# Performance work log

Hardware: AMD Instinct MI355X
Metric: run time of the kernel (lower is better)

Reference implementation:

```python
import jax, jax.numpy as jnp
import numpy as np

B, N, K1, M, D = 8, 4096, 17, 2, 256
NT = B * N          # total nodes
EPS = 1e-5          # PyG LayerNorm default eps


def setup_inputs() -> dict:
    key = jax.random.key(0)
    ks = jax.random.split(key, 13)
    s = 1.0 / np.sqrt(D)
    return {
        "x": jax.random.normal(ks[0], (NT, M, D), jnp.float32),
        "knn_edges": jax.random.randint(ks[1], (B, N, K1), 0, N),
        "edge_mask": jax.random.bernoulli(ks[2], 0.9, (B, N, K1)),
        "W0": jax.random.normal(ks[3], (D, D), jnp.float32) * s,
        "b0": jnp.zeros((D,), jnp.float32),
        "g0": jnp.ones((D,), jnp.float32),
        "be0": jnp.zeros((D,), jnp.float32),
        "a0": jnp.full((1,), 0.25, jnp.float32),
        "W1": jax.random.normal(ks[4], (D, D), jnp.float32) * s,
        "b1": jnp.zeros((D,), jnp.float32),
        "g1": jnp.ones((D,), jnp.float32),
        "be1": jnp.zeros((D,), jnp.float32),
        "a1": jnp.full((1,), 0.25, jnp.float32),
    }


def knn_to_edges(knn_edges, edge_mask):
    # drop self column 0, add per-graph batch offsets; keep fixed E with 0/1 weights
    e = knn_edges[:, :, 1:]                       # [B, N, K]
    m = edge_mask[:, :, 1:]
    off = (jnp.arange(B) * N)[:, None, None]      # [B,1,1]
    src = jnp.broadcast_to(jnp.arange(N)[None, :, None] + off, e.shape).reshape(-1)
    dst = (e + off).reshape(-1)
    w = m.reshape(-1).astype(jnp.float32)         # invalid edges -> weight 0
    return src, dst, w


def gcn_conv(h_in, W, b, src, dst, w):
    # PyG GCNConv: add self-loops (weight 1), symmetric normalization
    h = h_in @ W                                            # [NT, D]
    deg = jax.ops.segment_sum(w, dst, num_segments=NT) + 1.0
    dinv = jax.lax.rsqrt(deg)                               # [NT]
    norm = dinv[src] * w * dinv[dst]                        # [E]
    agg = jax.ops.segment_sum(norm[:, None] * h[src], dst, num_segments=NT)
    agg = agg + (dinv * dinv)[:, None] * h                  # self-loop term
    return agg + b


def graph_layernorm(x, g, b):
    # PyG LayerNorm mode='graph', batch=None: normalize over all nodes+features
    xc = x - jnp.mean(x)
    std = jnp.sqrt(jnp.mean(xc * xc))
    return g * (xc / (std + EPS)) + b


def prelu(x, a):
    return jnp.where(x >= 0, x, a * x)


def reference(x, knn_edges, edge_mask, W0, b0, g0, be0, a0, W1, b1, g1, be1, a1):
    src, dst, w = knn_to_edges(knn_edges, edge_mask)
    h = x[:, 0, :]                                          # [NT, D]
    for (W, b, g, be, a) in ((W0, b0, g0, be0, a0), (W1, b1, g1, be1, a1)):
        h = gcn_conv(h, W, b, src, dst, w)
        h = graph_layernorm(h, g, be)
        h = prelu(h, a)
    return h
```

## Files before the change

### kernel.cpp

```cpp
#include <hip/hip_runtime.h>
#include <hip/hip_bf16.h>
#include <stdint.h>

#define B_   8
#define N_   4096
#define K1_  17
#define D_   256
#define NT_  (B_*N_)
#define E16_ (NT_*16)
#define NP_  (NT_*D_)
#define EPS_ 1e-5f

typedef __attribute__((ext_vector_type(8))) short short8v;
typedef __attribute__((ext_vector_type(4))) short short4v;
typedef __attribute__((ext_vector_type(4))) float f32x4;

__device__ __forceinline__ unsigned short f2bfu(float f){
  unsigned u = __float_as_uint(f);
  unsigned r = (u + 0x7FFFu + ((u>>16)&1u)) >> 16;
  return (unsigned short)r;
}
__device__ __forceinline__ short f2bf(float f){ return (short)f2bfu(f); }
__device__ __forceinline__ unsigned pkbf(float lo, float hi){
  return (unsigned)f2bfu(lo) | ((unsigned)f2bfu(hi) << 16);
}
__device__ __forceinline__ float bf2f(short s){
  return __uint_as_float(((unsigned)(unsigned short)s) << 16);
}
__device__ __forceinline__ void unpack2(unsigned u, float& lo, float& hi){
  lo = __uint_as_float(u << 16);
  hi = __uint_as_float(u & 0xFFFF0000u);
}

__global__ __launch_bounds__(256) void k_prep(const float* __restrict__ W0,
                                              const float* __restrict__ W1,
                                              short* __restrict__ Wt0,
                                              short* __restrict__ Wt1,
                                              int* __restrict__ degcnt,
                                              const unsigned int* __restrict__ mw,
                                              int* __restrict__ flag){
  if (blockIdx.x < 128){
    const float* W  = (blockIdx.x & 1) ? W1  : W0;
    short*       Wt = (blockIdx.x & 1) ? Wt1 : Wt0;
    int tile = blockIdx.x >> 1;
    int ti = tile >> 3, tj = tile & 7;
    __shared__ float sm[32][33];
    int r = threadIdx.x >> 5, c = threadIdx.x & 31;
    #pragma unroll
    for (int i=0;i<4;i++)
      sm[r + i*8][c] = W[(ti*32 + r + i*8)*256 + tj*32 + c];
    __syncthreads();
    #pragma unroll
    for (int i=0;i<4;i++){
      int rr = r + i*8;
      Wt[(size_t)(tj*32 + rr)*256 + ti*32 + c] = f2bf(sm[c][rr]);
    }
  } else {
    int ib = blockIdx.x - 128;
    int i  = ib*256 + threadIdx.x;
    degcnt[i] = 0;
    if (ib == 0){
      __shared__ int s_int, s_f32;
      if (threadIdx.x==0){ s_int=1; s_f32=1; }
      __syncthreads();
      int bad_i=0, bad_f=0;
      #pragma unroll
      for (int j=0;j<4;j++){
        unsigned w = mw[threadIdx.x*4 + j];
        if (!(w==0u || w==1u))          bad_i=1;
        if (!(w==0u || w==0x3F800000u)) bad_f=1;
      }
      if (bad_i) atomicAnd(&s_int, 0);
      if (bad_f) atomicAnd(&s_f32, 0);
      __syncthreads();
      if (threadIdx.x==0) *flag = s_int ? 0 : (s_f32 ? 1 : 2);
    }
  }
}

__device__ __forceinline__ bool mask_at(const void* maskp, int f, int idx){
  if (f==0) return ((const int*)maskp)[idx] != 0;
  if (f==1) return ((const float*)maskp)[idx] != 0.0f;
  return ((const unsigned char*)maskp)[idx] != 0;
}

__global__ void k_deg(const int* __restrict__ knn, const void* __restrict__ maskp,
                      const int* __restrict__ flag, int* __restrict__ degcnt){
  int f = *flag;
  int e = blockIdx.x*blockDim.x + threadIdx.x;
  if (e >= E16_) return;
  int node = e >> 4;
  int k    = (e & 15) + 1;
  int idx  = node*K1_ + k;
  if (mask_at(maskp, f, idx)){
    int b   = node >> 12;
    int dst = knn[idx] + (b<<12);
    atomicAdd(&degcnt[dst], 1);
  }
}

__global__ void k_scan(const int* __restrict__ degcnt, int* __restrict__ rowptr,
                       int* __restrict__ fillptr, float* __restrict__ dinv){
  __shared__ int wsum[16];
  int t = threadIdx.x;
  int lane = t & 63, wid = t >> 6;
  int base = t*32;
  int loc[32]; int tot = 0;
  #pragma unroll
  for (int i=0;i<32;i++){ loc[i] = degcnt[base+i]; tot += loc[i]; }
  int inc = tot;
  #pragma unroll
  for (int off=1; off<64; off<<=1){
    int v = __shfl_up(inc, off, 64);
    if (lane >= off) inc += v;
  }
  if (lane == 63) wsum[wid] = inc;
  __syncthreads();
  int woff = 0;
  #pragma unroll
  for (int i=0;i<16;i++) if (i < wid) woff += wsum[i];
  int run = woff + inc - tot;
  #pragma unroll
  for (int i=0;i<32;i++){
    int v = base+i;
    rowptr[v]  = run;
    fillptr[v] = run;
    dinv[v]    = rsqrtf((float)loc[i] + 1.0f);
    run += loc[i];
  }
  if (t==1023) rowptr[NT_] = run;
}

__global__ __launch_bounds__(256, 3) void k_gemm_x_fill(const float* __restrict__ X,
                                                        const short* __restrict__ Wt,
                                                        short* __restrict__ C,
                                                        const int* __restrict__ knn,
                                                        const void* __restrict__ maskp,
                                                        const int* __restrict__ flag,
                                                        int* __restrict__ fillptr,
                                                        int* __restrict__ col){
  __shared__ short lA[128*64];
  __shared__ short lB[128*64];
  if (blockIdx.x >= 512){
    int f = *flag;
    int e = (blockIdx.x - 512)*256 + threadIdx.x;
    int node = e >> 4;
    int k    = (e & 15) + 1;
    int idx  = node*K1_ + k;
    if (mask_at(maskp, f, idx)){
      int b   = node >> 12;
      int dst = knn[idx] + (b<<12);
      int pos = atomicAdd(&fillptr[dst], 1);
      col[pos] = node;
    }
    return;
  }
  int lb     = (int)(blockIdx.x & 7)*64 + (int)(blockIdx.x >> 3);
  int rowblk = lb >> 1, half = lb & 1;
  int rowB = rowblk*128, colB = half*128;

  int t    = threadIdx.x;
  int wave = t >> 6, lane = t & 63;
  int lr   = lane & 15, qg = lane >> 4;
  int wr   = wave >> 1, wc = wave & 1;

  f32x4 acc[4][4];
  #pragma unroll
  for (int m=0;m<4;m++)
    #pragma unroll
    for (int n=0;n<4;n++) acc[m][n] = (f32x4){0.f,0.f,0.f,0.f};

  int srow[4], sch[4];
  #pragma unroll
  for (int i=0;i<4;i++){ int e = t + i*256; srow[i] = e>>3; sch[i] = e&7; }

  float4 rax[4], ray[4]; uint4 rb[4];
  #pragma unroll
  for (int i=0;i<4;i++){
    const float* ap = X + (size_t)(rowB+srow[i])*512 + sch[i]*8;
    rax[i] = *(const float4*)ap;
    ray[i] = *(const float4*)(ap+4);
    rb[i]  = *(const uint4*)(Wt + (size_t)(colB+srow[i])*256 + sch[i]*8);
  }

  for (int kc=0; kc<4; kc++){
    if (kc) __syncthreads();
    #pragma unroll
    for (int i=0;i<4;i++){
      int ph = srow[i]*8 + (sch[i] ^ (srow[i]&7));
      uint4 cv;
      cv.x = pkbf(rax[i].x, rax[i].y); cv.y = pkbf(rax[i].z, rax[i].w);
      cv.z = pkbf(ray[i].x, ray[i].y); cv.w = pkbf(ray[i].z, ray[i].w);
      *(uint4*)(lA + ph*8) = cv;
      *(uint4*)(lB + ph*8) = rb[i];
    }
    __syncthreads();
    if (kc < 3){
      #pragma unroll
      for (int i=0;i<4;i++){
        const float* ap = X + (size_t)(rowB+srow[i])*512 + (kc+1)*64 + sch[i]*8;
        rax[i] = *(const float4*)ap;
        ray[i] = *(const float4*)(ap+4);
        rb[i]  = *(const uint4*)(Wt + (size_t)(colB+srow[i])*256 + (kc+1)*64 + sch[i]*8);
      }
    }
    #pragma unroll
    for (int ks=0; ks<2; ks++){
      short8v af[4], bfr[4];
      #pragma unroll
      for (int m=0;m<4;m++){
        int row = wr*64 + m*16 + lr;
        af[m] = *(const short8v*)(lA + (row*8 + ((ks*4+qg) ^ (row&7)))*8);
      }
      #pragma unroll
      for (int n=0;n<4;n++){
        int coln = wc*64 + n*16 + lr;
        bfr[n] = *(const short8v*)(lB + (coln*8 + ((ks*4+qg) ^ (coln&7)))*8);
      }
      #pragma unroll
      for (int m=0;m<4;m++)
        #pragma unroll
        for (int n=0;n<4;n++)
          acc[m][n] = __builtin_amdgcn_mfma_f32_16x16x32_bf16(af[m], bfr[n], acc[m][n], 0, 0, 0);
    }
  }

  #pragma unroll
  for (int m=0;m<4;m++){
    int crow = rowB + wr*64 + m*16 + qg*4;
    #pragma unroll
    for (int n=0;n<4;n++){
      int ccol = colB + wc*64 + n*16 + lr;
      #pragma unroll
      for (int r=0;r<4;r++)
        C[(size_t)(crow + r)*256 + ccol] = f2bf(acc[m][n][r]);
    }
  }
}

__global__ __launch_bounds__(256, 3) void k_gemm_n(const unsigned* __restrict__ BaggU,
                                                   const float* __restrict__ g,
                                                   const float* __restrict__ be,
                                                   const float* __restrict__ aP,
                                                   const float* __restrict__ stats,
                                                   const short* __restrict__ Wt,
                                                   short* __restrict__ C){
  float mean = stats[0], inv = stats[1], a = aP[0];
  __shared__ short lA[128*64];
  __shared__ short lB[128*64];
  int lb     = (int)(blockIdx.x & 7)*64 + (int)(blockIdx.x >> 3);
  int rowblk = lb >> 1, half = lb & 1;
  int rowB = rowblk*128, colB = half*128;

  int t    = threadIdx.x;
  int wave = t >> 6, lane = t & 63;
  int lr   = lane & 15, qg = lane >> 4;
  int wr   = wave >> 1, wc = wave & 1;

  f32x4 acc[4][4];
  #pragma unroll
  for (int m=0;m<4;m++)
    #pragma unroll
    for (int n=0;n<4;n++) acc[m][n] = (f32x4){0.f,0.f,0.f,0.f};

  int srow[4], sch[4];
  #pragma unroll
  for (int i=0;i<4;i++){ int e = t + i*256; srow[i] = e>>3; sch[i] = e&7; }

  uint4 ra[4], rb[4];
  #pragma unroll
  for (int i=0;i<4;i++){
    ra[i] = *(const uint4*)(BaggU + (size_t)(rowB+srow[i])*128 + sch[i]*4);
    rb[i] = *(const uint4*)(Wt + (size_t)(colB+srow[i])*256 + sch[i]*8);
  }

  for (int kc=0; kc<4; kc++){
    if (kc) __syncthreads();
    #pragma unroll
    for (int i=0;i<4;i++){
      int ph = srow[i]*8 + (sch[i] ^ (srow[i]&7));
      int c0 = kc*64 + sch[i]*8;
      float4 g0 = *(const float4*)&g[c0],  g1 = *(const float4*)&g[c0+4];
      float4 e0 = *(const float4*)&be[c0], e1 = *(const float4*)&be[c0+4];
      float v[8];
      unpack2(ra[i].x, v[0], v[1]); unpack2(ra[i].y, v[2], v[3]);
      unpack2(ra[i].z, v[4], v[5]); unpack2(ra[i].w, v[6], v[7]);
      float gg[8] = {g0.x,g0.y,g0.z,g0.w,g1.x,g1.y,g1.z,g1.w};
      float eb[8] = {e0.x,e0.y,e0.z,e0.w,e1.x,e1.y,e1.z,e1.w};
      float o[8];
      #pragma unroll
      for (int j=0;j<8;j++){
        float tt = gg[j]*((v[j]-mean)*inv) + eb[j];
        o[j] = tt>=0.f ? tt : a*tt;
      }
      uint4 cv;
      cv.x = pkbf(o[0],o[1]); cv.y = pkbf(o[2],o[3]);
      cv.z = pkbf(o[4],o[5]); cv.w = pkbf(o[6],o[7]);
      *(uint4*)(lA + ph*8) = cv;
      *(uint4*)(lB + ph*8) = rb[i];
    }
    __syncthreads();
    if (kc < 3){
      #pragma unroll
      for (int i=0;i<4;i++){
        ra[i] = *(const uint4*)(BaggU + (size_t)(rowB+srow[i])*128 + (kc+1)*32 + sch[i]*4);
        rb[i] = *(const uint4*)(Wt + (size_t)(colB+srow[i])*256 + (kc+1)*64 + sch[i]*8);
      }
    }
    #pragma unroll
    for (int ks=0; ks<2; ks++){
      short8v af[4], bfr[4];
      #pragma unroll
      for (int m=0;m<4;m++){
        int row = wr*64 + m*16 + lr;
        af[m] = *(const short8v*)(lA + (row*8 + ((ks*4+qg) ^ (row&7)))*8);
      }
      #pragma unroll
      for (int n=0;n<4;n++){
        int coln = wc*64 + n*16 + lr;
        bfr[n] = *(const short8v*)(lB + (coln*8 + ((ks*4+qg) ^ (coln&7)))*8);
      }
      #pragma unroll
      for (int m=0;m<4;m++)
        #pragma unroll
        for (int n=0;n<4;n++)
          acc[m][n] = __builtin_amdgcn_mfma_f32_16x16x32_bf16(af[m], bfr[n], acc[m][n], 0, 0, 0);
    }
  }

  #pragma unroll
  for (int m=0;m<4;m++){
    int crow = rowB + wr*64 + m*16 + qg*4;
    #pragma unroll
    for (int n=0;n<4;n++){
      int ccol = colB + wc*64 + n*16 + lr;
      #pragma unroll
      for (int r=0;r<4;r++)
        C[(size_t)(crow + r)*256 + ccol] = f2bf(acc[m][n][r]);
    }
  }
}

__global__ __launch_bounds__(256) void k_agg(const short* __restrict__ Ab,
    const int* __restrict__ rowptr, const int* __restrict__ col,
    const float* __restrict__ dinv, const float* __restrict__ bvec,
    unsigned* __restrict__ outU, float* __restrict__ partS, float* __restrict__ partQ){
  int bid  = (int)(blockIdx.x & 7) * 512 + (int)(blockIdx.x >> 3);
  int node = bid*8 + (threadIdx.x >> 5);
  int sub  = threadIdx.x & 31;
  int c0   = sub*8;
  float dv = dinv[node];

  float acc[8];
  {
    short8v s = *(const short8v*)&Ab[(size_t)node*256 + c0];
    #pragma unroll
    for (int i=0;i<8;i++) acc[i] = dv * bf2f(s[i]);
  }
  int j0 = rowptr[node], j1 = rowptr[node+1];
  for (int base=j0; base<j1; base+=32){
    int n = j1 - base; n = n < 32 ? n : 32;
    int   myc = (sub < n) ? col[base+sub] : 0;
    float myd = (sub < n) ? dinv[myc]     : 0.f;
    for (int j=0;j<n;j++){
      int   s  = __shfl(myc, j, 32);
      float ds = __shfl(myd, j, 32);
      short8v nb = *(const short8v*)&Ab[(size_t)s*256 + c0];
      #pragma unroll
      for (int i=0;i<8;i++) acc[i] += ds * bf2f(nb[i]);
    }
  }
  float sum=0.f, sq=0.f;
  float o[8];
  #pragma unroll
  for (int i=0;i<8;i++){
    float v = dv*acc[i] + bvec[c0+i];
    o[i] = v;
    sum += v; sq += v*v;
  }
  uint4 ov;
  ov.x = pkbf(o[0],o[1]); ov.y = pkbf(o[2],o[3]);
  ov.z = pkbf(o[4],o[5]); ov.w = pkbf(o[6],o[7]);
  *(uint4*)&outU[(size_t)node*128 + sub*4] = ov;

  #pragma unroll
  for (int off=16; off>0; off>>=1){
    sum += __shfl_down(sum, off, 32);
    sq  += __shfl_down(sq,  off, 32);
  }
  __shared__ float ls1[8], ls2[8];
  if (sub==0){ ls1[threadIdx.x>>5]=sum; ls2[threadIdx.x>>5]=sq; }
  __syncthreads();
  if (threadIdx.x==0){
    float a=0.f, b=0.f;
    #pragma unroll
    for (int i=0;i<8;i++){ a+=ls1[i]; b+=ls2[i]; }
    partS[bid]=a; partQ[bid]=b;
  }
}

__global__ void k_stats(const float* __restrict__ partS, const float* __restrict__ partQ,
                        float* __restrict__ stats){
  __shared__ double s1[1024], s2[1024];
  int t = threadIdx.x;
  double a=0.0, b=0.0;
  for (int i=t; i<4096; i+=1024){ a += (double)partS[i]; b += (double)partQ[i]; }
  s1[t]=a; s2[t]=b; __syncthreads();
  for (int off=512; off>0; off>>=1){
    if (t<off){ s1[t]+=s1[t+off]; s2[t]+=s2[t+off]; }
    __syncthreads();
  }
  if (t==0){
    double mean = s1[0] / (double)NP_;
    double var  = s2[0] / (double)NP_ - mean*mean;
    var = var > 0.0 ? var : 0.0;
    stats[0] = (float)mean;
    stats[1] = (float)(1.0 / (sqrt(var) + (double)EPS_));
  }
}

__global__ __launch_bounds__(256) void k_norm_f32(const unsigned* __restrict__ inU,
    const float* __restrict__ g, const float* __restrict__ be,
    const float* __restrict__ aP, const float* __restrict__ stats,
    float* __restrict__ out){
  float mean = stats[0], inv = stats[1], a = aP[0];
  int gid   = blockIdx.x*256 + threadIdx.x;
  int base8 = gid*8;
  int c0    = base8 & (D_-1);
  uint4 vin = *(const uint4*)&inU[gid*4];
  float4 g0 = *(const float4*)&g[c0],  g1 = *(const float4*)&g[c0+4];
  float4 e0 = *(const float4*)&be[c0], e1 = *(const float4*)&be[c0+4];
  float v[8];
  unpack2(vin.x, v[0], v[1]); unpack2(vin.y, v[2], v[3]);
  unpack2(vin.z, v[4], v[5]); unpack2(vin.w, v[6], v[7]);
  float gg[8] = {g0.x,g0.y,g0.z,g0.w,g1.x,g1.y,g1.z,g1.w};
  float eb[8] = {e0.x,e0.y,e0.z,e0.w,e1.x,e1.y,e1.z,e1.w};
  f32x4 o0, o1;
  #pragma unroll
  for (int i=0;i<8;i++){
    float tt = gg[i]*((v[i]-mean)*inv) + eb[i];
    tt = tt>=0.f ? tt : a*tt;
    if (i<4) o0[i] = tt; else o1[i-4] = tt;
  }
  *(f32x4*)&out[base8]     = o0;
  *(f32x4*)&out[base8 + 4] = o1;
}


extern "C" void kernel_launch(void* const* d_in, const int* in_sizes, int n_in,
                              void* d_out, int out_size, void* d_ws, size_t ws_size,
                              hipStream_t stream){
  const float* x    = (const float*)d_in[0];
  const int*   knn  = (const int*)  d_in[1];
  const void*  mask =               d_in[2];
  const float* W0   = (const float*)d_in[3];
  const float* b0   = (const float*)d_in[4];
  const float* g0   = (const float*)d_in[5];
  const float* be0  = (const float*)d_in[6];
  const float* a0   = (const float*)d_in[7];
  const float* W1   = (const float*)d_in[8];
  const float* b1   = (const float*)d_in[9];
  const float* g1   = (const float*)d_in[10];
  const float* be1  = (const float*)d_in[11];
  const float* a1   = (const float*)d_in[12];
  float* out = (float*)d_out;

  char* w = (char*)d_ws;
  size_t off = 0;
  auto alloc = [&](size_t bytes)->void*{
    void* p = w + off; off = (off + bytes + 255) & ~(size_t)255; return p;
  };
  int*      degcnt  = (int*)     alloc(NT_*4);
  int*      rowptr  = (int*)     alloc((NT_+1)*4);
  int*      fillptr = (int*)     alloc(NT_*4);
  int*      col     = (int*)     alloc(E16_*4);
  float*    dinv    = (float*)   alloc(NT_*4);
  float*    partS   = (float*)   alloc(4096*4);
  float*    partQ   = (float*)   alloc(4096*4);
  float*    stats   = (float*)   alloc(4*4);
  int*      flag    = (int*)     alloc(4);
  short*    Ab      = (short*)   alloc((size_t)NP_*2);
  unsigned* Bagg    = (unsigned*)alloc((size_t)NP_*2);
  short*    Wt0     = (short*)   alloc(256*256*2);
  short*    Wt1     = (short*)   alloc(256*256*2);

  hipLaunchKernelGGL(k_prep,  dim3(256),      dim3(256), 0, stream, W0, W1, Wt0, Wt1,
                     degcnt, (const unsigned int*)mask, flag);
  hipLaunchKernelGGL(k_deg,   dim3(E16_/256), dim3(256), 0, stream, knn, mask, flag, degcnt);
  hipLaunchKernelGGL(k_scan,  dim3(1),        dim3(1024),0, stream, degcnt, rowptr, fillptr, dinv);

  hipLaunchKernelGGL(k_gemm_x_fill, dim3(2560), dim3(256), 0, stream, x, Wt0, Ab,
                     knn, mask, flag, fillptr, col);
  hipLaunchKernelGGL(k_agg,    dim3(NT_/8),   dim3(256), 0, stream, Ab, rowptr, col, dinv, b0, Bagg, partS, partQ);
  hipLaunchKernelGGL(k_stats,  dim3(1),       dim3(1024),0, stream, partS, partQ, stats);

  hipLaunchKernelGGL(k_gemm_n, dim3(512),     dim3(256), 0, stream, Bagg, g0, be0, a0, stats, Wt1, Ab);
  hipLaunchKernelGGL(k_agg,    dim3(NT_/8),   dim3(256), 0, stream, Ab, rowptr, col, dinv, b1, Bagg, partS, partQ);
  hipLaunchKernelGGL(k_stats,  dim3(1),       dim3(1024),0, stream, partS, partQ, stats);
  hipLaunchKernelGGL(k_norm_f32, dim3(NP_/2048), dim3(256), 0, stream, Bagg, g1, be1, a1, stats, out);
}
```

Before: 159.8 us.

## Use 512-thread GEMM blocks and stage bf16 output through LDS for coalesced stores

```diff
diff --git a/kernel.cpp b/kernel.cpp
--- a/kernel.cpp
+++ b/kernel.cpp
@@ -131,7 +131,7 @@
   if (t==1023) rowptr[NT_] = run;
 }
 
-__global__ __launch_bounds__(256, 3) void k_gemm_x_fill(const float* __restrict__ X,
+__global__ __launch_bounds__(512, 4) void k_gemm_x_fill(const float* __restrict__ X,
                                                         const short* __restrict__ Wt,
                                                         short* __restrict__ C,
                                                         const int* __restrict__ knn,
@@ -139,11 +139,10 @@
                                                         const int* __restrict__ flag,
                                                         int* __restrict__ fillptr,
                                                         int* __restrict__ col){
-  __shared__ short lA[128*64];
-  __shared__ short lB[128*64];
+  __shared__ short lds[2*128*64];
   if (blockIdx.x >= 512){
     int f = *flag;
-    int e = (blockIdx.x - 512)*256 + threadIdx.x;
+    int e = (int)(blockIdx.x - 512)*512 + threadIdx.x;
     int node = e >> 4;
     int k    = (e & 15) + 1;
     int idx  = node*K1_ + k;
@@ -155,6 +154,8 @@
     }
     return;
   }
+  short* lA = lds;
+  short* lB = lds + 128*64;
   int lb     = (int)(blockIdx.x & 7)*64 + (int)(blockIdx.x >> 3);
   int rowblk = lb >> 1, half = lb & 1;
   int rowB = rowblk*128, colB = half*128;
@@ -162,21 +163,21 @@
   int t    = threadIdx.x;
   int wave = t >> 6, lane = t & 63;
   int lr   = lane & 15, qg = lane >> 4;
-  int wr   = wave >> 1, wc = wave & 1;
-
-  f32x4 acc[4][4];
+  int wr   = wave >> 2, wc = wave & 3;
+
+  f32x4 acc[4][2];
   #pragma unroll
   for (int m=0;m<4;m++)
     #pragma unroll
-    for (int n=0;n<4;n++) acc[m][n] = (f32x4){0.f,0.f,0.f,0.f};
-
-  int srow[4], sch[4];
-  #pragma unroll
-  for (int i=0;i<4;i++){ int e = t + i*256; srow[i] = e>>3; sch[i] = e&7; }
-
-  float4 rax[4], ray[4]; uint4 rb[4];
-  #pragma unroll
-  for (int i=0;i<4;i++){
+    for (int n=0;n<2;n++) acc[m][n] = (f32x4){0.f,0.f,0.f,0.f};
+
+  int srow[2], sch[2];
+  #pragma unroll
+  for (int i=0;i<2;i++){ int e = t + i*512; srow[i] = e>>3; sch[i] = e&7; }
+
+  float4 rax[2], ray[2]; uint4 rb[2];
+  #pragma unroll
+  for (int i=0;i<2;i++){
     const float* ap = X + (size_t)(rowB+srow[i])*512 + sch[i]*8;
     rax[i] = *(const float4*)ap;
     ray[i] = *(const float4*)(ap+4);
@@ -186,7 +187,7 @@
   for (int kc=0; kc<4; kc++){
     if (kc) __syncthreads();
     #pragma unroll
-    for (int i=0;i<4;i++){
+    for (int i=0;i<2;i++){
       int ph = srow[i]*8 + (sch[i] ^ (srow[i]&7));
       uint4 cv;
       cv.x = pkbf(rax[i].x, rax[i].y); cv.y = pkbf(rax[i].z, rax[i].w);
@@ -197,7 +198,7 @@
     __syncthreads();
     if (kc < 3){
       #pragma unroll
-      for (int i=0;i<4;i++){
+      for (int i=0;i<2;i++){
         const float* ap = X + (size_t)(rowB+srow[i])*512 + (kc+1)*64 + sch[i]*8;
         rax[i] = *(const float4*)ap;
         ray[i] = *(const float4*)(ap+4);
@@ -206,39 +207,51 @@
     }
     #pragma unroll
     for (int ks=0; ks<2; ks++){
-      short8v af[4], bfr[4];
+      short8v af[4], bfr[2];
       #pragma unroll
       for (int m=0;m<4;m++){
         int row = wr*64 + m*16 + lr;
         af[m] = *(const short8v*)(lA + (row*8 + ((ks*4+qg) ^ (row&7)))*8);
       }
       #pragma unroll
-      for (int n=0;n<4;n++){
-        int coln = wc*64 + n*16 + lr;
+      for (int n=0;n<2;n++){
+        int coln = wc*32 + n*16 + lr;
         bfr[n] = *(const short8v*)(lB + (coln*8 + ((ks*4+qg) ^ (coln&7)))*8);
       }
       #pragma unroll
       for (int m=0;m<4;m++)
         #pragma unroll
-        for (int n=0;n<4;n++)
+        for (int n=0;n<2;n++)
           acc[m][n] = __builtin_amdgcn_mfma_f32_16x16x32_bf16(af[m], bfr[n], acc[m][n], 0, 0, 0);
     }
   }
 
+  __syncthreads();
   #pragma unroll
   for (int m=0;m<4;m++){
-    int crow = rowB + wr*64 + m*16 + qg*4;
-    #pragma unroll
-    for (int n=0;n<4;n++){
-      int ccol = colB + wc*64 + n*16 + lr;
-      #pragma unroll
-      for (int r=0;r<4;r++)
-        C[(size_t)(crow + r)*256 + ccol] = f2bf(acc[m][n][r]);
-    }
-  }
-}
-
-__global__ __launch_bounds__(256, 3) void k_gemm_n(const unsigned* __restrict__ BaggU,
+    int rloc = wr*64 + m*16 + qg*4;
+    #pragma unroll
+    for (int n=0;n<2;n++){
+      int cloc = wc*32 + n*16 + lr;
+      int cch  = cloc >> 3, cin = cloc & 7;
+      #pragma unroll
+      for (int r=0;r<4;r++){
+        int row = rloc + r;
+        lds[row*128 + ((cch ^ (row&7))<<3) + cin] = f2bf(acc[m][n][r]);
+      }
+    }
+  }
+  __syncthreads();
+  #pragma unroll
+  for (int i=0;i<4;i++){
+    int e = t + i*512;
+    int row = e >> 4, chunk = e & 15;
+    uint4 v = *(const uint4*)(lds + row*128 + ((chunk ^ (row&7))<<3));
+    *(uint4*)(C + (size_t)(rowB+row)*256 + colB + chunk*8) = v;
+  }
+}
+
+__global__ __launch_bounds__(512, 4) void k_gemm_n(const unsigned* __restrict__ BaggU,
                                                    const float* __restrict__ g,
                                                    const float* __restrict__ be,
                                                    const float* __restrict__ aP,
@@ -246,8 +259,9 @@
                                                    const short* __restrict__ Wt,
                                                    short* __restrict__ C){
   float mean = stats[0], inv = stats[1], a = aP[0];
-  __shared__ short lA[128*64];
-  __shared__ short lB[128*64];
+  __shared__ short lds[2*128*64];
+  short* lA = lds;
+  short* lB = lds + 128*64;
   int lb     = (int)(blockIdx.x & 7)*64 + (int)(blockIdx.x >> 3);
   int rowblk = lb >> 1, half = lb & 1;
   int rowB = rowblk*128, colB = half*128;
@@ -255,21 +269,21 @@
   int t    = threadIdx.x;
   int wave = t >> 6, lane = t & 63;
   int lr   = lane & 15, qg = lane >> 4;
-  int wr   = wave >> 1, wc = wave & 1;
-
-  f32x4 acc[4][4];
+  int wr   = wave >> 2, wc = wave & 3;
+
+  f32x4 acc[4][2];
   #pragma unroll
   for (int m=0;m<4;m++)
     #pragma unroll
-    for (int n=0;n<4;n++) acc[m][n] = (f32x4){0.f,0.f,0.f,0.f};
-
-  int srow[4], sch[4];
-  #pragma unroll
-  for (int i=0;i<4;i++){ int e = t + i*256; srow[i] = e>>3; sch[i] = e&7; }
-
-  uint4 ra[4], rb[4];
-  #pragma unroll
-  for (int i=0;i<4;i++){
+    for (int n=0;n<2;n++) acc[m][n] = (f32x4){0.f,0.f,0.f,0.f};
+
+  int srow[2], sch[2];
+  #pragma unroll
+  for (int i=0;i<2;i++){ int e = t + i*512; srow[i] = e>>3; sch[i] = e&7; }
+
+  uint4 ra[2], rb[2];
+  #pragma unroll
+  for (int i=0;i<2;i++){
     ra[i] = *(const uint4*)(BaggU + (size_t)(rowB+srow[i])*128 + sch[i]*4);
     rb[i] = *(const uint4*)(Wt + (size_t)(colB+srow[i])*256 + sch[i]*8);
   }
@@ -277,7 +291,7 @@
   for (int kc=0; kc<4; kc++){
     if (kc) __syncthreads();
     #pragma unroll
-    for (int i=0;i<4;i++){
+    for (int i=0;i<2;i++){
       int ph = srow[i]*8 + (sch[i] ^ (srow[i]&7));
       int c0 = kc*64 + sch[i]*8;
       float4 g0 = *(const float4*)&g[c0],  g1 = *(const float4*)&g[c0+4];
@@ -302,42 +316,54 @@
     __syncthreads();
     if (kc < 3){
       #pragma unroll
-      for (int i=0;i<4;i++){
+      for (int i=0;i<2;i++){
         ra[i] = *(const uint4*)(BaggU + (size_t)(rowB+srow[i])*128 + (kc+1)*32 + sch[i]*4);
         rb[i] = *(const uint4*)(Wt + (size_t)(colB+srow[i])*256 + (kc+1)*64 + sch[i]*8);
       }
     }
     #pragma unroll
     for (int ks=0; ks<2; ks++){
-      short8v af[4], bfr[4];
+      short8v af[4], bfr[2];
       #pragma unroll
       for (int m=0;m<4;m++){
         int row = wr*64 + m*16 + lr;
         af[m] = *(const short8v*)(lA + (row*8 + ((ks*4+qg) ^ (row&7)))*8);
       }
       #pragma unroll
-      for (int n=0;n<4;n++){
-        int coln = wc*64 + n*16 + lr;
+      for (int n=0;n<2;n++){
+        int coln = wc*32 + n*16 + lr;
         bfr[n] = *(const short8v*)(lB + (coln*8 + ((ks*4+qg) ^ (coln&7)))*8);
       }
       #pragma unroll
       for (int m=0;m<4;m++)
         #pragma unroll
-        for (int n=0;n<4;n++)
+        for (int n=0;n<2;n++)
           acc[m][n] = __builtin_amdgcn_mfma_f32_16x16x32_bf16(af[m], bfr[n], acc[m][n], 0, 0, 0);
     }
   }
 
+  __syncthreads();
   #pragma unroll
   for (int m=0;m<4;m++){
-    int crow = rowB + wr*64 + m*16 + qg*4;
-    #pragma unroll
-    for (int n=0;n<4;n++){
-      int ccol = colB + wc*64 + n*16 + lr;
-      #pragma unroll
-      for (int r=0;r<4;r++)
-        C[(size_t)(crow + r)*256 + ccol] = f2bf(acc[m][n][r]);
-    }
+    int rloc = wr*64 + m*16 + qg*4;
+    #pragma unroll
+    for (int n=0;n<2;n++){
+      int cloc = wc*32 + n*16 + lr;
+      int cch  = cloc >> 3, cin = cloc & 7;
+      #pragma unroll
+      for (int r=0;r<4;r++){
+        int row = rloc + r;
+        lds[row*128 + ((cch ^ (row&7))<<3) + cin] = f2bf(acc[m][n][r]);
+      }
+    }
+  }
+  __syncthreads();
+  #pragma unroll
+  for (int i=0;i<4;i++){
+    int e = t + i*512;
+    int row = e >> 4, chunk = e & 15;
+    uint4 v = *(const uint4*)(lds + row*128 + ((chunk ^ (row&7))<<3));
+    *(uint4*)(C + (size_t)(rowB+row)*256 + colB + chunk*8) = v;
   }
 }
 
@@ -489,12 +515,12 @@
   hipLaunchKernelGGL(k_deg,   dim3(E16_/256), dim3(256), 0, stream, knn, mask, flag, degcnt);
   hipLaunchKernelGGL(k_scan,  dim3(1),        dim3(1024),0, stream, degcnt, rowptr, fillptr, dinv);
 
-  hipLaunchKernelGGL(k_gemm_x_fill, dim3(2560), dim3(256), 0, stream, x, Wt0, Ab,
+  hipLaunchKernelGGL(k_gemm_x_fill, dim3(1536), dim3(512), 0, stream, x, Wt0, Ab,
                      knn, mask, flag, fillptr, col);
   hipLaunchKernelGGL(k_agg,    dim3(NT_/8),   dim3(256), 0, stream, Ab, rowptr, col, dinv, b0, Bagg, partS, partQ);
   hipLaunchKernelGGL(k_stats,  dim3(1),       dim3(1024),0, stream, partS, partQ, stats);
 
-  hipLaunchKernelGGL(k_gemm_n, dim3(512),     dim3(256), 0, stream, Bagg, g0, be0, a0, stats, Wt1, Ab);
+  hipLaunchKernelGGL(k_gemm_n, dim3(512),     dim3(512), 0, stream, Bagg, g0, be0, a0, stats, Wt1, Ab);
   hipLaunchKernelGGL(k_agg,    dim3(NT_/8),   dim3(256), 0, stream, Ab, rowptr, col, dinv, b1, Bagg, partS, partQ);
   hipLaunchKernelGGL(k_stats,  dim3(1),       dim3(1024),0, stream, partS, partQ, stats);
   hipLaunchKernelGGL(k_norm_f32, dim3(NP_/2048), dim3(256), 0, stream, Bagg, g1, be1, a1, stats, out);
```

After: 161.4 us. Within noise of the previous version (+1.0%).

## Fuse graph-norm stats reduction into consumers and widen GEMM tiles to full N

Applied to the files above, without the earlier changes.

```diff
diff --git a/kernel.cpp b/kernel.cpp
--- a/kernel.cpp
+++ b/kernel.cpp
@@ -12,7 +12,6 @@
 #define EPS_ 1e-5f
 
 typedef __attribute__((ext_vector_type(8))) short short8v;
-typedef __attribute__((ext_vector_type(4))) short short4v;
 typedef __attribute__((ext_vector_type(4))) float f32x4;
 
 __device__ __forceinline__ unsigned short f2bfu(float f){
@@ -131,7 +130,47 @@
   if (t==1023) rowptr[NT_] = run;
 }
 
-__global__ __launch_bounds__(256, 3) void k_gemm_x_fill(const float* __restrict__ X,
+__device__ __forceinline__ void g_mfma4(const short* lA, const short* lB,
+                                        int wr, int wc, int lr, int qg,
+                                        f32x4 (&acc)[4][4]){
+  #pragma unroll
+  for (int ks=0; ks<2; ks++){
+    short8v af[4], bfr[4];
+    #pragma unroll
+    for (int m=0;m<4;m++){
+      int row = wr*64 + m*16 + lr;
+      af[m] = *(const short8v*)(lA + (row*8 + ((ks*4+qg) ^ (row&7)))*8);
+    }
+    #pragma unroll
+    for (int n=0;n<4;n++){
+      int coln = wc*64 + n*16 + lr;
+      bfr[n] = *(const short8v*)(lB + (coln*8 + ((ks*4+qg) ^ (coln&7)))*8);
+    }
+    #pragma unroll
+    for (int m=0;m<4;m++)
+      #pragma unroll
+      for (int n=0;n<4;n++)
+        acc[m][n] = __builtin_amdgcn_mfma_f32_16x16x32_bf16(af[m], bfr[n], acc[m][n], 0, 0, 0);
+  }
+}
+
+__device__ __forceinline__ void g_cstore(short* __restrict__ C, int rowB,
+                                         int wr, int wc, int lr, int qg,
+                                         const f32x4 (&acc)[4][4]){
+  #pragma unroll
+  for (int m=0;m<4;m++){
+    int crow = rowB + wr*64 + m*16 + qg*4;
+    #pragma unroll
+    for (int n=0;n<4;n++){
+      int ccol = wc*64 + n*16 + lr;
+      #pragma unroll
+      for (int r=0;r<4;r++)
+        C[(size_t)(crow + r)*256 + ccol] = f2bf(acc[m][n][r]);
+    }
+  }
+}
+
+__global__ __launch_bounds__(512, 4) void k_gemm_x_fill(const float* __restrict__ X,
                                                         const short* __restrict__ Wt,
                                                         short* __restrict__ C,
                                                         const int* __restrict__ knn,
@@ -140,10 +179,10 @@
                                                         int* __restrict__ fillptr,
                                                         int* __restrict__ col){
   __shared__ short lA[128*64];
-  __shared__ short lB[128*64];
-  if (blockIdx.x >= 512){
+  __shared__ short lB[256*64];
+  if (blockIdx.x >= 256){
     int f = *flag;
-    int e = (blockIdx.x - 512)*256 + threadIdx.x;
+    int e = (int)(blockIdx.x - 256)*512 + threadIdx.x;
     int node = e >> 4;
     int k    = (e & 15) + 1;
     int idx  = node*K1_ + k;
@@ -155,14 +194,13 @@
     }
     return;
   }
-  int lb     = (int)(blockIdx.x & 7)*64 + (int)(blockIdx.x >> 3);
-  int rowblk = lb >> 1, half = lb & 1;
-  int rowB = rowblk*128, colB = half*128;
+  int lb   = (int)(blockIdx.x & 7)*32 + (int)(blockIdx.x >> 3);
+  int rowB = lb*128;
 
   int t    = threadIdx.x;
   int wave = t >> 6, lane = t & 63;
   int lr   = lane & 15, qg = lane >> 4;
-  int wr   = wave >> 1, wc = wave & 1;
+  int wr   = wave >> 2, wc = wave & 3;
 
   f32x4 acc[4][4];
   #pragma unroll
@@ -170,92 +208,98 @@
     #pragma unroll
     for (int n=0;n<4;n++) acc[m][n] = (f32x4){0.f,0.f,0.f,0.f};
 
-  int srow[4], sch[4];
-  #pragma unroll
-  for (int i=0;i<4;i++){ int e = t + i*256; srow[i] = e>>3; sch[i] = e&7; }
-
-  float4 rax[4], ray[4]; uint4 rb[4];
-  #pragma unroll
-  for (int i=0;i<4;i++){
-    const float* ap = X + (size_t)(rowB+srow[i])*512 + sch[i]*8;
+  int saA[2], scA[2], saB[4], scB[4];
+  #pragma unroll
+  for (int i=0;i<2;i++){ int e = t + i*512; saA[i] = e>>3; scA[i] = e&7; }
+  #pragma unroll
+  for (int i=0;i<4;i++){ int e = t + i*512; saB[i] = e>>3; scB[i] = e&7; }
+
+  float4 rax[2], ray[2]; uint4 rb[4];
+  #pragma unroll
+  for (int i=0;i<2;i++){
+    const float* ap = X + (size_t)(rowB+saA[i])*512 + scA[i]*8;
     rax[i] = *(const float4*)ap;
     ray[i] = *(const float4*)(ap+4);
-    rb[i]  = *(const uint4*)(Wt + (size_t)(colB+srow[i])*256 + sch[i]*8);
-  }
+  }
+  #pragma unroll
+  for (int i=0;i<4;i++)
+    rb[i] = *(const uint4*)(Wt + (size_t)saB[i]*256 + scB[i]*8);
 
   for (int kc=0; kc<4; kc++){
     if (kc) __syncthreads();
     #pragma unroll
-    for (int i=0;i<4;i++){
-      int ph = srow[i]*8 + (sch[i] ^ (srow[i]&7));
+    for (int i=0;i<2;i++){
+      int ph = saA[i]*8 + (scA[i] ^ (saA[i]&7));
       uint4 cv;
       cv.x = pkbf(rax[i].x, rax[i].y); cv.y = pkbf(rax[i].z, rax[i].w);
       cv.z = pkbf(ray[i].x, ray[i].y); cv.w = pkbf(ray[i].z, ray[i].w);
       *(uint4*)(lA + ph*8) = cv;
+    }
+    #pragma unroll
+    for (int i=0;i<4;i++){
+      int ph = saB[i]*8 + (scB[i] ^ (saB[i]&7));
       *(uint4*)(lB + ph*8) = rb[i];
     }
     __syncthreads();
     if (kc < 3){
       #pragma unroll
-      for (int i=0;i<4;i++){
-        const float* ap = X + (size_t)(rowB+srow[i])*512 + (kc+1)*64 + sch[i]*8;
+      for (int i=0;i<2;i++){
+        const float* ap = X + (size_t)(rowB+saA[i])*512 + (kc+1)*64 + scA[i]*8;
         rax[i] = *(const float4*)ap;
         ray[i] = *(const float4*)(ap+4);
-        rb[i]  = *(const uint4*)(Wt + (size_t)(colB+srow[i])*256 + (kc+1)*64 + sch[i]*8);
       }
-    }
-    #pragma unroll
-    for (int ks=0; ks<2; ks++){
-      short8v af[4], bfr[4];
-      #pragma unroll
-      for (int m=0;m<4;m++){
-        int row = wr*64 + m*16 + lr;
-        af[m] = *(const short8v*)(lA + (row*8 + ((ks*4+qg) ^ (row&7)))*8);
-      }
-      #pragma unroll
-      for (int n=0;n<4;n++){
-        int coln = wc*64 + n*16 + lr;
-        bfr[n] = *(const short8v*)(lB + (coln*8 + ((ks*4+qg) ^ (coln&7)))*8);
-      }
-      #pragma unroll
-      for (int m=0;m<4;m++)
-        #pragma unroll
-        for (int n=0;n<4;n++)
-          acc[m][n] = __builtin_amdgcn_mfma_f32_16x16x32_bf16(af[m], bfr[n], acc[m][n], 0, 0, 0);
-    }
-  }
-
-  #pragma unroll
-  for (int m=0;m<4;m++){
-    int crow = rowB + wr*64 + m*16 + qg*4;
-    #pragma unroll
-    for (int n=0;n<4;n++){
-      int ccol = colB + wc*64 + n*16 + lr;
-      #pragma unroll
-      for (int r=0;r<4;r++)
-        C[(size_t)(crow + r)*256 + ccol] = f2bf(acc[m][n][r]);
-    }
-  }
-}
-
-__global__ __launch_bounds__(256, 3) void k_gemm_n(const unsigned* __restrict__ BaggU,
+      #pragma unroll
+      for (int i=0;i<4;i++)
+        rb[i] = *(const uint4*)(Wt + (size_t)saB[i]*256 + (kc+1)*64 + scB[i]*8);
+    }
+    g_mfma4(lA, lB, wr, wc, lr, qg, acc);
+  }
+  g_cstore(C, rowB, wr, wc, lr, qg, acc);
+}
+
+__global__ __launch_bounds__(512, 4) void k_gemm_n(const unsigned* __restrict__ BaggU,
                                                    const float* __restrict__ g,
                                                    const float* __restrict__ be,
                                                    const float* __restrict__ aP,
-                                                   const float* __restrict__ stats,
+                                                   const float* __restrict__ partS,
+                                                   const float* __restrict__ partQ,
                                                    const short* __restrict__ Wt,
                                                    short* __restrict__ C){
-  float mean = stats[0], inv = stats[1], a = aP[0];
   __shared__ short lA[128*64];
-  __shared__ short lB[128*64];
-  int lb     = (int)(blockIdx.x & 7)*64 + (int)(blockIdx.x >> 3);
-  int rowblk = lb >> 1, half = lb & 1;
-  int rowB = rowblk*128, colB = half*128;
+  __shared__ short lB[256*64];
+  float mean, inv;
+  {
+    double* sS = (double*)lA;
+    double* sQ = (double*)(lA + 4096);
+    double a=0.0, b=0.0;
+    for (int i=threadIdx.x; i<4096; i+=512){ a += (double)partS[i]; b += (double)partQ[i]; }
+    sS[threadIdx.x]=a; sQ[threadIdx.x]=b;
+    __syncthreads();
+    for (int off=256; off>0; off>>=1){
+      if ((int)threadIdx.x < off){ sS[threadIdx.x]+=sS[threadIdx.x+off]; sQ[threadIdx.x]+=sQ[threadIdx.x+off]; }
+      __syncthreads();
+    }
+    if (threadIdx.x==0){
+      double m   = sS[0] / (double)NP_;
+      double var = sQ[0] / (double)NP_ - m*m;
+      var = var > 0.0 ? var : 0.0;
+      ((float*)lA)[0] = (float)m;
+      ((float*)lA)[1] = (float)(1.0 / (sqrt(var) + (double)EPS_));
+    }
+    __syncthreads();
+    mean = ((float*)lA)[0];
+    inv  = ((float*)lA)[1];
+    __syncthreads();
+  }
+  float a = aP[0];
+
+  int lb   = (int)(blockIdx.x & 7)*32 + (int)(blockIdx.x >> 3);
+  int rowB = lb*128;
 
   int t    = threadIdx.x;
   int wave = t >> 6, lane = t & 63;
   int lr   = lane & 15, qg = lane >> 4;
-  int wr   = wave >> 1, wc = wave & 1;
+  int wr   = wave >> 2, wc = wave & 3;
 
   f32x4 acc[4][4];
   #pragma unroll
@@ -263,23 +307,26 @@
     #pragma unroll
     for (int n=0;n<4;n++) acc[m][n] = (f32x4){0.f,0.f,0.f,0.f};
 
-  int srow[4], sch[4];
-  #pragma unroll
-  for (int i=0;i<4;i++){ int e = t + i*256; srow[i] = e>>3; sch[i] = e&7; }
-
-  uint4 ra[4], rb[4];
-  #pragma unroll
-  for (int i=0;i<4;i++){
-    ra[i] = *(const uint4*)(BaggU + (size_t)(rowB+srow[i])*128 + sch[i]*4);
-    rb[i] = *(const uint4*)(Wt + (size_t)(colB+srow[i])*256 + sch[i]*8);
-  }
+  int saA[2], scA[2], saB[4], scB[4];
+  #pragma unroll
+  for (int i=0;i<2;i++){ int e = t + i*512; saA[i] = e>>3; scA[i] = e&7; }
+  #pragma unroll
+  for (int i=0;i<4;i++){ int e = t + i*512; saB[i] = e>>3; scB[i] = e&7; }
+
+  uint4 ra[2], rb[4];
+  #pragma unroll
+  for (int i=0;i<2;i++)
+    ra[i] = *(const uint4*)(BaggU + (size_t)(rowB+saA[i])*128 + scA[i]*4);
+  #pragma unroll
+  for (int i=0;i<4;i++)
+    rb[i] = *(const uint4*)(Wt + (size_t)saB[i]*256 + scB[i]*8);
 
   for (int kc=0; kc<4; kc++){
     if (kc) __syncthreads();
     #pragma unroll
-    for (int i=0;i<4;i++){
-      int ph = srow[i]*8 + (sch[i] ^ (srow[i]&7));
-      int c0 = kc*64 + sch[i]*8;
+    for (int i=0;i<2;i++){
+      int ph = saA[i]*8 + (scA[i] ^ (saA[i]&7));
+      int c0 = kc*64 + scA[i]*8;
       float4 g0 = *(const float4*)&g[c0],  g1 = *(const float4*)&g[c0+4];
       float4 e0 = *(const float4*)&be[c0], e1 = *(const float4*)&be[c0+4];
       float v[8];
@@ -297,48 +344,24 @@
       cv.x = pkbf(o[0],o[1]); cv.y = pkbf(o[2],o[3]);
       cv.z = pkbf(o[4],o[5]); cv.w = pkbf(o[6],o[7]);
       *(uint4*)(lA + ph*8) = cv;
+    }
+    #pragma unroll
+    for (int i=0;i<4;i++){
+      int ph = saB[i]*8 + (scB[i] ^ (saB[i]&7));
       *(uint4*)(lB + ph*8) = rb[i];
     }
     __syncthreads();
     if (kc < 3){
       #pragma unroll
-      for (int i=0;i<4;i++){
-        ra[i] = *(const uint4*)(BaggU + (size_t)(rowB+srow[i])*128 + (kc+1)*32 + sch[i]*4);
-        rb[i] = *(const uint4*)(Wt + (size_t)(colB+srow[i])*256 + (kc+1)*64 + sch[i]*8);
-      }
-    }
-    #pragma unroll
-    for (int ks=0; ks<2; ks++){
-      short8v af[4], bfr[4];
-      #pragma unroll
-      for (int m=0;m<4;m++){
-        int row = wr*64 + m*16 + lr;
-        af[m] = *(const short8v*)(lA + (row*8 + ((ks*4+qg) ^ (row&7)))*8);
-      }
-      #pragma unroll
-      for (int n=0;n<4;n++){
-        int coln = wc*64 + n*16 + lr;
-        bfr[n] = *(const short8v*)(lB + (coln*8 + ((ks*4+qg) ^ (coln&7)))*8);
-      }
-      #pragma unroll
-      for (int m=0;m<4;m++)
-        #pragma unroll
-        for (int n=0;n<4;n++)
-          acc[m][n] = __builtin_amdgcn_mfma_f32_16x16x32_bf16(af[m], bfr[n], acc[m][n], 0, 0, 0);
-    }
-  }
-
-  #pragma unroll
-  for (int m=0;m<4;m++){
-    int crow = rowB + wr*64 + m*16 + qg*4;
-    #pragma unroll
-    for (int n=0;n<4;n++){
-      int ccol = colB + wc*64 + n*16 + lr;
-      #pragma unroll
-      for (int r=0;r<4;r++)
-        C[(size_t)(crow + r)*256 + ccol] = f2bf(acc[m][n][r]);
-    }
-  }
+      for (int i=0;i<2;i++)
+        ra[i] = *(const uint4*)(BaggU + (size_t)(rowB+saA[i])*128 + (kc+1)*32 + scA[i]*4);
+      #pragma unroll
+      for (int i=0;i<4;i++)
+        rb[i] = *(const uint4*)(Wt + (size_t)saB[i]*256 + (kc+1)*64 + scB[i]*8);
+    }
+    g_mfma4(lA, lB, wr, wc, lr, qg, acc);
+  }
+  g_cstore(C, rowB, wr, wc, lr, qg, acc);
 }
 
 __global__ __launch_bounds__(256) void k_agg(const short* __restrict__ Ab,
@@ -399,51 +422,54 @@
   }
 }
 
-__global__ void k_stats(const float* __restrict__ partS, const float* __restrict__ partQ,
-                        float* __restrict__ stats){
-  __shared__ double s1[1024], s2[1024];
-  int t = threadIdx.x;
-  double a=0.0, b=0.0;
-  for (int i=t; i<4096; i+=1024){ a += (double)partS[i]; b += (double)partQ[i]; }
-  s1[t]=a; s2[t]=b; __syncthreads();
-  for (int off=512; off>0; off>>=1){
-    if (t<off){ s1[t]+=s1[t+off]; s2[t]+=s2[t+off]; }
-    __syncthreads();
-  }
-  if (t==0){
-    double mean = s1[0] / (double)NP_;
-    double var  = s2[0] / (double)NP_ - mean*mean;
-    var = var > 0.0 ? var : 0.0;
-    stats[0] = (float)mean;
-    stats[1] = (float)(1.0 / (sqrt(var) + (double)EPS_));
-  }
-}
-
 __global__ __launch_bounds__(256) void k_norm_f32(const unsigned* __restrict__ inU,
     const float* __restrict__ g, const float* __restrict__ be,
-    const float* __restrict__ aP, const float* __restrict__ stats,
-    float* __restrict__ out){
-  float mean = stats[0], inv = stats[1], a = aP[0];
-  int gid   = blockIdx.x*256 + threadIdx.x;
-  int base8 = gid*8;
-  int c0    = base8 & (D_-1);
-  uint4 vin = *(const uint4*)&inU[gid*4];
-  float4 g0 = *(const float4*)&g[c0],  g1 = *(const float4*)&g[c0+4];
-  float4 e0 = *(const float4*)&be[c0], e1 = *(const float4*)&be[c0+4];
-  float v[8];
-  unpack2(vin.x, v[0], v[1]); unpack2(vin.y, v[2], v[3]);
-  unpack2(vin.z, v[4], v[5]); unpack2(vin.w, v[6], v[7]);
-  float gg[8] = {g0.x,g0.y,g0.z,g0.w,g1.x,g1.y,g1.z,g1.w};
-  float eb[8] = {e0.x,e0.y,e0.z,e0.w,e1.x,e1.y,e1.z,e1.w};
-  f32x4 o0, o1;
-  #pragma unroll
-  for (int i=0;i<8;i++){
-    float tt = gg[i]*((v[i]-mean)*inv) + eb[i];
-    tt = tt>=0.f ? tt : a*tt;
-    if (i<4) o0[i] = tt; else o1[i-4] = tt;
-  }
-  *(f32x4*)&out[base8]     = o0;
-  *(f32x4*)&out[base8 + 4] = o1;
+    const float* __restrict__ aP, const float* __restrict__ partS,
+    const float* __restrict__ partQ, float* __restrict__ out){
+  __shared__ double sS[256], sQ[256];
+  __shared__ float s_mean, s_inv;
+  {
+    double a=0.0, b=0.0;
+    for (int i=threadIdx.x; i<4096; i+=256){ a += (double)partS[i]; b += (double)partQ[i]; }
+    sS[threadIdx.x]=a; sQ[threadIdx.x]=b;
+    __syncthreads();
+    for (int off=128; off>0; off>>=1){
+      if ((int)threadIdx.x < off){ sS[threadIdx.x]+=sS[threadIdx.x+off]; sQ[threadIdx.x]+=sQ[threadIdx.x+off]; }
+      __syncthreads();
+    }
+    if (threadIdx.x==0){
+      double m   = sS[0] / (double)NP_;
+      double var = sQ[0] / (double)NP_ - m*m;
+      var = var > 0.0 ? var : 0.0;
+      s_mean = (float)m;
+      s_inv  = (float)(1.0 / (sqrt(var) + (double)EPS_));
+    }
+    __syncthreads();
+  }
+  float mean = s_mean, inv = s_inv, a = aP[0];
+  #pragma unroll
+  for (int it=0; it<4; it++){
+    int gid   = it*(1024*256) + blockIdx.x*256 + threadIdx.x;
+    int base8 = gid*8;
+    int c0    = base8 & (D_-1);
+    uint4 vin = *(const uint4*)&inU[gid*4];
+    float4 g0 = *(const float4*)&g[c0],  g1 = *(const float4*)&g[c0+4];
+    float4 e0 = *(const float4*)&be[c0], e1 = *(const float4*)&be[c0+4];
+    float v[8];
+    unpack2(vin.x, v[0], v[1]); unpack2(vin.y, v[2], v[3]);
+    unpack2(vin.z, v[4], v[5]); unpack2(vin.w, v[6], v[7]);
+    float gg[8] = {g0.x,g0.y,g0.z,g0.w,g1.x,g1.y,g1.z,g1.w};
+    float eb[8] = {e0.x,e0.y,e0.z,e0.w,e1.x,e1.y,e1.z,e1.w};
+    f32x4 o0, o1;
+    #pragma unroll
+    for (int i=0;i<8;i++){
+      float tt = gg[i]*((v[i]-mean)*inv) + eb[i];
+      tt = tt>=0.f ? tt : a*tt;
+      if (i<4) o0[i] = tt; else o1[i-4] = tt;
+    }
+    *(f32x4*)&out[base8]     = o0;
+    *(f32x4*)&out[base8 + 4] = o1;
+  }
 }
 
 
@@ -477,7 +503,6 @@
   float*    dinv    = (float*)   alloc(NT_*4);
   float*    partS   = (float*)   alloc(4096*4);
   float*    partQ   = (float*)   alloc(4096*4);
-  float*    stats   = (float*)   alloc(4*4);
   int*      flag    = (int*)     alloc(4);
   short*    Ab      = (short*)   alloc((size_t)NP_*2);
   unsigned* Bagg    = (unsigned*)alloc((size_t)NP_*2);
@@ -489,13 +514,13 @@
   hipLaunchKernelGGL(k_deg,   dim3(E16_/256), dim3(256), 0, stream, knn, mask, flag, degcnt);
   hipLaunchKernelGGL(k_scan,  dim3(1),        dim3(1024),0, stream, degcnt, rowptr, fillptr, dinv);
 
-  hipLaunchKernelGGL(k_gemm_x_fill, dim3(2560), dim3(256), 0, stream, x, Wt0, Ab,
+  hipLaunchKernelGGL(k_gemm_x_fill, dim3(1280), dim3(512), 0, stream, x, Wt0, Ab,
                      knn, mask, flag, fillptr, col);
   hipLaunchKernelGGL(k_agg,    dim3(NT_/8),   dim3(256), 0, stream, Ab, rowptr, col, dinv, b0, Bagg, partS, partQ);
-  hipLaunchKernelGGL(k_stats,  dim3(1),       dim3(1024),0, stream, partS, partQ, stats);
-
-  hipLaunchKernelGGL(k_gemm_n, dim3(512),     dim3(256), 0, stream, Bagg, g0, be0, a0, stats, Wt1, Ab);
+
+  hipLaunchKernelGGL(k_gemm_n, dim3(256),     dim3(512), 0, stream, Bagg, g0, be0, a0,
+                     partS, partQ, Wt1, Ab);
   hipLaunchKernelGGL(k_agg,    dim3(NT_/8),   dim3(256), 0, stream, Ab, rowptr, col, dinv, b1, Bagg, partS, partQ);
-  hipLaunchKernelGGL(k_stats,  dim3(1),       dim3(1024),0, stream, partS, partQ, stats);
-  hipLaunchKernelGGL(k_norm_f32, dim3(NP_/2048), dim3(256), 0, stream, Bagg, g1, be1, a1, stats, out);
-}
+  hipLaunchKernelGGL(k_norm_f32, dim3(1024),  dim3(256), 0, stream, Bagg, g1, be1, a1,
+                     partS, partQ, out);
+}
```

Result: slower. 163.8 us (+2.5%).
